# Optimization experiments

Hardware: AMD Instinct MI355X
Metric: run time of the kernel (lower is better)

## Reference

```python
import jax, jax.numpy as jnp
import numpy as np

B, T, N, F_IN, F_OUT = 8, 16, 512, 128, 64
NEG_INF = -9e15


def setup_inputs() -> dict:
    key = jax.random.key(0)
    k1, k2, k3, k4, k5 = jax.random.split(key, 5)
    x = jax.random.normal(k1, (B, T, N, F_IN), dtype=jnp.float32)
    # nn.Linear weights: FC_W [out, in], FC_a [1, 2*out], no bias
    W = jax.random.normal(k2, (F_OUT, F_IN), dtype=jnp.float32) * 0.05
    a = jax.random.normal(k3, (1, 2 * F_OUT), dtype=jnp.float32) * 0.05
    adj = jax.random.randint(k4, (N, N), 0, 2, dtype=jnp.int32)
    adj_we = jax.random.uniform(k5, (N, N), dtype=jnp.float32)
    return {"x": x, "W": W, "a": a, "adj": adj, "adj_we": adj_we}


def reference(x, W, a, adj, adj_we):
    fout = W.shape[0]
    # h = FC_W(input): [B,T,N,Fout]
    h = jnp.einsum("btnf,of->btno", x, W)
    # Additive GAT score decomposition: e[i,j] = LeakyReLU(a1.h_i + a2.h_j)
    # (equivalent to FC_a(cat([h_i, h_j])) without materializing [B,T,N,N,2F])
    a1 = a[0, :fout]
    a2 = a[0, fout:]
    src = jnp.einsum("btno,o->btn", h, a1)  # contribution of node i (repeated rows)
    dst = jnp.einsum("btno,o->btn", h, a2)  # contribution of node j (tiled rows)
    e = jax.nn.leaky_relu(src[..., :, None] + dst[..., None, :], negative_slope=0.01)
    # mask where adj <= 0, scale by edge weights, softmax over neighbors (dim=3)
    att = jnp.where(adj > 0, e, NEG_INF)
    att = att * adj_we
    att = jax.nn.softmax(att, axis=-1)
    # h_prime = attention @ h : [B,T,N,N] @ [B,T,N,Fout]
    return jnp.einsum("btij,btjo->btio", att, h)
```

## Files before the change

### kernel.cpp

```cpp
#include <hip/hip_runtime.h>
#include <hip/hip_bf16.h>

#define BTOT 128
#define NN   512
#define FIN  128
#define FOUT 64

typedef __attribute__((ext_vector_type(8))) short bf16x8;
typedef __attribute__((ext_vector_type(4))) float f32x4;

static __device__ inline ushort f2bf(float f) {
    __hip_bfloat16 h = __float2bfloat16(f);
    return *(ushort*)&h;
}
static __device__ inline float bf2f(ushort u) {
    uint v = (uint)u << 16;
    return __uint_as_float(v);
}

__global__ void k_prep(const float* __restrict__ W, const int* __restrict__ adj,
                       const float* __restrict__ we, ushort* __restrict__ Whi,
                       ushort* __restrict__ Wlo, ushort* __restrict__ cds) {
    int b = blockIdx.x;
    if (b >= 256) {
        int i = (b - 256) * 256 + threadIdx.x;
        float w = W[i];
        ushort hi = f2bf(w);
        Whi[i] = hi;
        Wlo[i] = f2bf(w - bf2f(hi));
        return;
    }
    int lin = (b * 256 + threadIdx.x) * 4;
    int i = lin >> 9, j0 = lin & 511;
    int4   a4 = *(const int4*)&adj[lin];
    float4 w4 = *(const float4*)&we[lin];
    ushort o[4];
#pragma unroll
    for (int e = 0; e < 4; ++e) {
        bool  cn = ((const int*)&a4)[e] > 0;
        float w  = ((const float*)&w4)[e];
        if (cn) {
            uint ub = __float_as_uint(w * 1.44269504f);
            uint tt = ub + 0xFFFFu + ((ub >> 17) & 1u);
            o[e] = (ushort)(((tt >> 17) << 1) | 1u);
        } else {
            o[e] = (w > 0.f) ? (ushort)0 : (ushort)1;
        }
    }
    int swz = ((((i >> 4) * 2 + (j0 >> 8)) * 8 + ((j0 >> 5) & 7)) << 9)
            + (((j0 >> 3) & 3) << 7) + ((i & 15) << 3) + (j0 & 7);
    *(uint2*)&cds[swz] = *(uint2*)&o[0];
}

__global__ void k_feat(const float* __restrict__ x, const ushort* __restrict__ Whi,
                       const ushort* __restrict__ Wlo, const float* __restrict__ a,
                       ushort* __restrict__ ht, float* __restrict__ srcv,
                       float* __restrict__ dstv) {
    const int t    = threadIdx.x;
    const int bid  = blockIdx.x;
    const int bt   = bid & 127;
    const int nt   = bid >> 7;
    const int wv   = t >> 6, lane = t & 63;
    const int r    = lane & 15;
    const int kc   = lane >> 4;
    const int n0   = nt * 64 + wv * 16;

    const float* xrow = x + ((long)bt * NN + n0 + r) * FIN;

    f32x4 acc[4] = {{0,0,0,0},{0,0,0,0},{0,0,0,0},{0,0,0,0}};

#pragma unroll
    for (int ks = 0; ks < 4; ++ks) {
        f32x4 xa = __builtin_nontemporal_load((const f32x4*)&xrow[ks * 32 + kc * 8]);
        f32x4 xb = __builtin_nontemporal_load((const f32x4*)&xrow[ks * 32 + kc * 8 + 4]);
        float xv[8] = {xa[0], xa[1], xa[2], xa[3], xb[0], xb[1], xb[2], xb[3]};
        bf16x8 Ahi, Alo;
#pragma unroll
        for (int e = 0; e < 8; ++e) {
            uint b = __float_as_uint(xv[e]);
            float hf = __uint_as_float(b & 0xFFFF0000u);
            Ahi[e] = (short)(b >> 16);
            float rr = xv[e] - hf;
            Alo[e] = (short)(__float_as_uint(rr) >> 16);
        }
#pragma unroll
        for (int g = 0; g < 4; ++g) {
            const int wo = (g * 16 + r) * FIN + ks * 32 + kc * 8;
            bf16x8 Bhi = *(const bf16x8*)&Whi[wo];
            bf16x8 Blo = *(const bf16x8*)&Wlo[wo];
            acc[g] = __builtin_amdgcn_mfma_f32_16x16x32_bf16(Ahi, Bhi, acc[g], 0, 0, 0);
            acc[g] = __builtin_amdgcn_mfma_f32_16x16x32_bf16(Alo, Bhi, acc[g], 0, 0, 0);
            acc[g] = __builtin_amdgcn_mfma_f32_16x16x32_bf16(Ahi, Blo, acc[g], 0, 0, 0);
        }
    }

    float a1g[4], a2g[4];
#pragma unroll
    for (int g = 0; g < 4; ++g) {
        a1g[g] = a[g * 16 + r];
        a2g[g] = a[FOUT + g * 16 + r];
    }
    f32x4 s1v = {0,0,0,0}, s2v = {0,0,0,0};
#pragma unroll
    for (int g = 0; g < 4; ++g)
#pragma unroll
        for (int reg = 0; reg < 4; ++reg) {
            s1v[reg] += acc[g][reg] * a1g[g];
            s2v[reg] += acc[g][reg] * a2g[g];
        }
#pragma unroll
    for (int off = 8; off; off >>= 1)
#pragma unroll
        for (int reg = 0; reg < 4; ++reg) {
            s1v[reg] += __shfl_down(s1v[reg], off, 16);
            s2v[reg] += __shfl_down(s2v[reg], off, 16);
        }
    if (r == 0) {
        float4 o1 = make_float4(s1v[0], s1v[1], s1v[2], s1v[3]);
        float4 o2 = make_float4(s2v[0], s2v[1], s2v[2], s2v[3]);
        *(float4*)&srcv[bt * NN + n0 + kc * 4] = o1;
        *(float4*)&dstv[bt * NN + n0 + kc * 4] = o2;
    }

#pragma unroll
    for (int g = 0; g < 4; ++g) {
        uint2 pk;
        pk.x = (uint)f2bf(acc[g][0]) | ((uint)f2bf(acc[g][1]) << 16);
        pk.y = (uint)f2bf(acc[g][2]) | ((uint)f2bf(acc[g][3]) << 16);
        *(uint2*)&ht[(long)bt * (FOUT * NN) + (g * 16 + r) * NN + n0 + kc * 4] = pk;
    }
}

static __device__ inline bf16x8 make_afrag(uint4 c, float4 d0, float4 d1, float si) {
    float dv[8] = {d0.x, d0.y, d0.z, d0.w, d1.x, d1.y, d1.z, d1.w};
    uint  cw[4] = {c.x, c.y, c.z, c.w};
    union { uint u[4]; bf16x8 v; } A;
#pragma unroll
    for (int q = 0; q < 4; ++q) {
        uint u = cw[q];
        float c0 = __uint_as_float((u << 16) & 0xFFFE0000u);
        float c1 = __uint_as_float(u & 0xFFFE0000u);
        float s0 = si + dv[2 * q],     lr0 = fmaxf(s0, 0.01f * s0);
        float s1 = si + dv[2 * q + 1], lr1 = fmaxf(s1, 0.01f * s1);
        float p0 = __builtin_amdgcn_exp2f(c0 * lr0);
        float p1 = __builtin_amdgcn_exp2f(c1 * lr1);
        p0 = (u & 1u)       ? p0 : 0.f;
        p1 = (u & 0x10000u) ? p1 : 0.f;
        A.u[q] = __builtin_amdgcn_perm(__float_as_uint(p1), __float_as_uint(p0),
                                       0x07060302u);
    }
    return A.v;
}

__global__ __launch_bounds__(256, 4)
void k_attn(const ushort* __restrict__ ht, const float* __restrict__ srcv,
            const float* __restrict__ dstv, const ushort* __restrict__ cds,
            float* __restrict__ out) {
    __shared__ ushort hs[64 * 256];
    __shared__ float dst_s[NN];

    const int t    = threadIdx.x;
    const int bid  = blockIdx.x;
    const int bt   = bid & 127;
    const int it   = bid >> 7;
    const int i0   = it << 6;
    const int lane = t & 63;
    const int wv   = t >> 6;
    const int r16  = lane & 15;
    const int kc   = lane >> 4;
    const int koff = kc * 8;
    const int xr   = r16 & 7;

    const int ri = i0 + wv * 16 + r16;
    const float si = srcv[bt * NN + ri];
    const ushort* cdb = cds + (((it * 4 + wv) * 2) << 12) + (lane << 3);
    const ushort* htb = ht + (long)bt * (FOUT * NN);

    for (int q = t; q < NN; q += 256) dst_s[q] = dstv[bt * NN + q];

    f32x4 ac0 = {0,0,0,0}, ac1 = {0,0,0,0}, ac2 = {0,0,0,0}, ac3 = {0,0,0,0},
          acd = {0,0,0,0};
    bf16x8 ones;
#pragma unroll
    for (int j = 0; j < 8; ++j) ones[j] = (short)0x3F80;

#pragma unroll
    for (int half = 0; half < 2; ++half) {
        uint4 cdv[8];
#pragma unroll
        for (int f = 0; f < 8; ++f)
            cdv[f] = *(const uint4*)&cdb[(half * 8 + f) << 9];

        __syncthreads();
#pragma unroll
        for (int q = 0; q < 8; ++q) {
            int idx = q * 256 + t;
            int o = idx >> 5, c8 = idx & 31;
            float4 v = *(const float4*)&htb[(o << 9) + (half << 8) + (c8 << 3)];
            *(float4*)&hs[(o << 8) + ((c8 ^ (o & 7)) << 3)] = v;
        }
        __syncthreads();

        const int jg = half * 256;
#pragma unroll
        for (int jtl = 0; jtl < 4; ++jtl) {
            const int jgc = jg + jtl * 64;
            float4 d00 = *(float4*)&dst_s[jgc + koff];
            float4 d01 = *(float4*)&dst_s[jgc + koff + 4];
            float4 d10 = *(float4*)&dst_s[jgc + 32 + koff];
            float4 d11 = *(float4*)&dst_s[jgc + 32 + koff + 4];

            bf16x8 A0 = make_afrag(cdv[2 * jtl],     d00, d01, si);
            bf16x8 A1 = make_afrag(cdv[2 * jtl + 1], d10, d11, si);

#pragma unroll
            for (int s2 = 0; s2 < 2; ++s2) {
                bf16x8 A = s2 ? A1 : A0;
                const int c8v = jtl * 8 + s2 * 4 + kc;
                const int cs  = (c8v ^ xr) << 3;
                bf16x8 b0 = *(bf16x8*)&hs[(( 0 + r16) << 8) + cs];
                bf16x8 b1 = *(bf16x8*)&hs[((16 + r16) << 8) + cs];
                bf16x8 b2 = *(bf16x8*)&hs[((32 + r16) << 8) + cs];
                bf16x8 b3 = *(bf16x8*)&hs[((48 + r16) << 8) + cs];
                __builtin_amdgcn_s_setprio(1);
                ac0 = __builtin_amdgcn_mfma_f32_16x16x32_bf16(A, b0, ac0, 0, 0, 0);
                ac1 = __builtin_amdgcn_mfma_f32_16x16x32_bf16(A, b1, ac1, 0, 0, 0);
                ac2 = __builtin_amdgcn_mfma_f32_16x16x32_bf16(A, b2, ac2, 0, 0, 0);
                ac3 = __builtin_amdgcn_mfma_f32_16x16x32_bf16(A, b3, ac3, 0, 0, 0);
                acd = __builtin_amdgcn_mfma_f32_16x16x32_bf16(A, ones, acd, 0, 0, 0);
                __builtin_amdgcn_s_setprio(0);
            }
        }
    }

    float* ob = out + ((long)bt * NN + i0 + wv * 16) * FOUT;
#pragma unroll
    for (int reg = 0; reg < 4; ++reg) {
        float inv = 1.0f / acd[reg];
        const int rw = (kc * 4 + reg) * FOUT + r16;
        __builtin_nontemporal_store(ac0[reg] * inv, &ob[rw +  0]);
        __builtin_nontemporal_store(ac1[reg] * inv, &ob[rw + 16]);
        __builtin_nontemporal_store(ac2[reg] * inv, &ob[rw + 32]);
        __builtin_nontemporal_store(ac3[reg] * inv, &ob[rw + 48]);
    }
}

extern "C" void kernel_launch(void* const* d_in, const int* in_sizes, int n_in,
                              void* d_out, int out_size, void* d_ws, size_t ws_size,
                              hipStream_t stream) {
    const float* x      = (const float*)d_in[0];
    const float* W      = (const float*)d_in[1];
    const float* a      = (const float*)d_in[2];
    const int*   adj    = (const int*)d_in[3];
    const float* adj_we = (const float*)d_in[4];
    float* out = (float*)d_out;

    ushort* Whi  = (ushort*)d_ws;
    ushort* Wlo  = Whi + FOUT * FIN;
    ushort* ht   = Wlo + FOUT * FIN;
    float*  srcv = (float*)(ht + BTOT * FOUT * NN);
    float*  dstv = srcv + BTOT * NN;
    ushort* cdsw = (ushort*)(dstv + BTOT * NN);

    hipLaunchKernelGGL(k_prep, dim3(288), dim3(256), 0, stream,
                       W, adj, adj_we, Whi, Wlo, cdsw);
    hipLaunchKernelGGL(k_feat, dim3(1024), dim3(256), 0, stream,
                       x, Whi, Wlo, a, ht, srcv, dstv);
    hipLaunchKernelGGL(k_attn, dim3(1024), dim3(256), 0, stream,
                       ht, srcv, dstv, cdsw, out);
}
```

Measured before the change: 46.57 us.

## Double-buffer h tiles in LDS via direct global-to-LDS loads across four stages

Splits the 512-column key loop into four 128-column stages with two LDS buffers. The next h tile is prefetched using global_load_lds (direct global-to-LDS, no register round trip) and the next adjacency/coefficient fragments are prefetched into registers while MFMAs run on the current buffer. The goal is to hide global load latency behind compute and shrink LDS use. It adds one barrier per stage and more live registers, and the XOR swizzle now happens on the global source addresses.

```diff
diff --git a/kernel.cpp b/kernel.cpp
--- a/kernel.cpp
+++ b/kernel.cpp
@@ -16,6 +16,12 @@
 static __device__ inline float bf2f(ushort u) {
     uint v = (uint)u << 16;
     return __uint_as_float(v);
+}
+
+static __device__ inline void gll16(const ushort* gsrc, ushort* ldst) {
+    __builtin_amdgcn_global_load_lds(
+        (const __attribute__((address_space(1))) uint*)gsrc,
+        (__attribute__((address_space(3))) uint*)ldst, 16, 0, 0);
 }
 
 __global__ void k_prep(const float* __restrict__ W, const int* __restrict__ adj,
@@ -156,7 +162,7 @@
 void k_attn(const ushort* __restrict__ ht, const float* __restrict__ srcv,
             const float* __restrict__ dstv, const ushort* __restrict__ cds,
             float* __restrict__ out) {
-    __shared__ ushort hs[64 * 256];
+    __shared__ ushort hs[2][64 * 128];
     __shared__ float dst_s[NN];
 
     const int t    = threadIdx.x;
@@ -176,6 +182,9 @@
     const ushort* cdb = cds + (((it * 4 + wv) * 2) << 12) + (lane << 3);
     const ushort* htb = ht + (long)bt * (FOUT * NN);
 
+    const int so  = t >> 4;
+    const int sgs = t & 15;
+
     for (int q = t; q < NN; q += 256) dst_s[q] = dstv[bt * NN + q];
 
     f32x4 ac0 = {0,0,0,0}, ac1 = {0,0,0,0}, ac2 = {0,0,0,0}, ac3 = {0,0,0,0},
@@ -184,44 +193,56 @@
 #pragma unroll
     for (int j = 0; j < 8; ++j) ones[j] = (short)0x3F80;
 
-#pragma unroll
-    for (int half = 0; half < 2; ++half) {
-        uint4 cdv[8];
-#pragma unroll
-        for (int f = 0; f < 8; ++f)
-            cdv[f] = *(const uint4*)&cdb[(half * 8 + f) << 9];
-
-        __syncthreads();
-#pragma unroll
-        for (int q = 0; q < 8; ++q) {
-            int idx = q * 256 + t;
-            int o = idx >> 5, c8 = idx & 31;
-            float4 v = *(const float4*)&htb[(o << 9) + (half << 8) + (c8 << 3)];
-            *(float4*)&hs[(o << 8) + ((c8 ^ (o & 7)) << 3)] = v;
-        }
-        __syncthreads();
-
-        const int jg = half * 256;
-#pragma unroll
-        for (int jtl = 0; jtl < 4; ++jtl) {
-            const int jgc = jg + jtl * 64;
-            float4 d00 = *(float4*)&dst_s[jgc + koff];
-            float4 d01 = *(float4*)&dst_s[jgc + koff + 4];
-            float4 d10 = *(float4*)&dst_s[jgc + 32 + koff];
-            float4 d11 = *(float4*)&dst_s[jgc + 32 + koff + 4];
-
-            bf16x8 A0 = make_afrag(cdv[2 * jtl],     d00, d01, si);
-            bf16x8 A1 = make_afrag(cdv[2 * jtl + 1], d10, d11, si);
+    uint4 cdc[4], cdn[4];
+#pragma unroll
+    for (int f = 0; f < 4; ++f) cdc[f] = *(const uint4*)&cdb[f << 9];
+
+#pragma unroll
+    for (int q = 0; q < 4; ++q) {
+        int idx = q * 256 + t;
+        int o = idx >> 4, gs = idx & 15;
+        gll16(htb + (o << 9) + ((gs ^ (o & 7)) << 3),
+              &hs[0][(q * 256 + (t & 0xC0)) * 8]);
+    }
+    __syncthreads();
+
+#pragma unroll
+    for (int qt = 0; qt < 4; ++qt) {
+        const int cur = qt & 1;
+
+        if (qt < 3) {
+#pragma unroll
+            for (int f = 0; f < 4; ++f)
+                cdn[f] = *(const uint4*)&cdb[(4 * (qt + 1) + f) << 9];
+#pragma unroll
+            for (int q = 0; q < 4; ++q) {
+                int idx = q * 256 + t;
+                int o = idx >> 4, gs = idx & 15;
+                gll16(htb + (o << 9) + ((qt + 1) << 7) + ((gs ^ (o & 7)) << 3),
+                      &hs[cur ^ 1][(q * 256 + (t & 0xC0)) * 8]);
+            }
+        }
+
+#pragma unroll
+        for (int j2 = 0; j2 < 2; ++j2) {
+            const int jb = qt * 128 + j2 * 64;
+            float4 d00 = *(float4*)&dst_s[jb + koff];
+            float4 d01 = *(float4*)&dst_s[jb + koff + 4];
+            float4 d10 = *(float4*)&dst_s[jb + 32 + koff];
+            float4 d11 = *(float4*)&dst_s[jb + 32 + koff + 4];
+
+            bf16x8 A0 = make_afrag(cdc[2 * j2],     d00, d01, si);
+            bf16x8 A1 = make_afrag(cdc[2 * j2 + 1], d10, d11, si);
 
 #pragma unroll
             for (int s2 = 0; s2 < 2; ++s2) {
                 bf16x8 A = s2 ? A1 : A0;
-                const int c8v = jtl * 8 + s2 * 4 + kc;
-                const int cs  = (c8v ^ xr) << 3;
-                bf16x8 b0 = *(bf16x8*)&hs[(( 0 + r16) << 8) + cs];
-                bf16x8 b1 = *(bf16x8*)&hs[((16 + r16) << 8) + cs];
-                bf16x8 b2 = *(bf16x8*)&hs[((32 + r16) << 8) + cs];
-                bf16x8 b3 = *(bf16x8*)&hs[((48 + r16) << 8) + cs];
+                const int g = j2 * 8 + s2 * 4 + kc;
+                const int cs = ((g ^ xr) << 3);
+                bf16x8 b0 = *(bf16x8*)&hs[cur][(( 0 + r16) << 7) + cs];
+                bf16x8 b1 = *(bf16x8*)&hs[cur][((16 + r16) << 7) + cs];
+                bf16x8 b2 = *(bf16x8*)&hs[cur][((32 + r16) << 7) + cs];
+                bf16x8 b3 = *(bf16x8*)&hs[cur][((48 + r16) << 7) + cs];
                 __builtin_amdgcn_s_setprio(1);
                 ac0 = __builtin_amdgcn_mfma_f32_16x16x32_bf16(A, b0, ac0, 0, 0, 0);
                 ac1 = __builtin_amdgcn_mfma_f32_16x16x32_bf16(A, b1, ac1, 0, 0, 0);
@@ -231,6 +252,10 @@
                 __builtin_amdgcn_s_setprio(0);
             }
         }
+
+        __syncthreads();
+#pragma unroll
+        for (int f = 0; f < 4; ++f) cdc[f] = cdn[f];
     }
 
     float* ob = out + ((long)bt * NN + i0 + wv * 16) * FOUT;
```

Measured after the change: 46.59 us. About the same (+0.0%).

## Fold adjacency preprocessing into feature kernel and hoist x loads ahead of MFMAs

Applied to the files above, without the earlier changes.

The adjacency/edge-weight encoding moves out of the prep kernel and into extra blocks of the feature kernel. That leaves only a tiny W split kernel on the critical path, and the adjacency work overlaps with the feature GEMM. The feature kernel now issues all x loads up front as ordinary cached loads instead of nontemporal ones, and converts them to bf16 hi/lo before the MFMA loop. It also gains launch bounds of 256 threads with 4 blocks. The cost is higher register pressure and a branch in k_feat that separates the two block roles.

```diff
diff --git a/kernel.cpp b/kernel.cpp
--- a/kernel.cpp
+++ b/kernel.cpp
@@ -18,46 +18,48 @@
     return __uint_as_float(v);
 }
 
-__global__ void k_prep(const float* __restrict__ W, const int* __restrict__ adj,
-                       const float* __restrict__ we, ushort* __restrict__ Whi,
-                       ushort* __restrict__ Wlo, ushort* __restrict__ cds) {
-    int b = blockIdx.x;
-    if (b >= 256) {
-        int i = (b - 256) * 256 + threadIdx.x;
-        float w = W[i];
-        ushort hi = f2bf(w);
-        Whi[i] = hi;
-        Wlo[i] = f2bf(w - bf2f(hi));
+__global__ void k_prep_w(const float* __restrict__ W, ushort* __restrict__ Whi,
+                         ushort* __restrict__ Wlo) {
+    int i = blockIdx.x * 256 + threadIdx.x;
+    float w = W[i];
+    ushort hi = f2bf(w);
+    Whi[i] = hi;
+    Wlo[i] = f2bf(w - bf2f(hi));
+}
+
+__global__ __launch_bounds__(256, 4)
+void k_feat(const float* __restrict__ x, const ushort* __restrict__ Whi,
+            const ushort* __restrict__ Wlo, const float* __restrict__ a,
+            ushort* __restrict__ ht, float* __restrict__ srcv,
+            float* __restrict__ dstv, const int* __restrict__ adj,
+            const float* __restrict__ we, ushort* __restrict__ cds) {
+    const int t   = threadIdx.x;
+    const int bid = blockIdx.x;
+
+    if (bid >= 1024) {
+        int lin = ((bid - 1024) * 256 + t) * 4;
+        int i = lin >> 9, j0 = lin & 511;
+        int4   a4 = *(const int4*)&adj[lin];
+        float4 w4 = *(const float4*)&we[lin];
+        ushort o[4];
+#pragma unroll
+        for (int e = 0; e < 4; ++e) {
+            bool  cn = ((const int*)&a4)[e] > 0;
+            float w  = ((const float*)&w4)[e];
+            if (cn) {
+                uint ub = __float_as_uint(w * 1.44269504f);
+                uint tt = ub + 0xFFFFu + ((ub >> 17) & 1u);
+                o[e] = (ushort)(((tt >> 17) << 1) | 1u);
+            } else {
+                o[e] = (w > 0.f) ? (ushort)0 : (ushort)1;
+            }
+        }
+        int swz = ((((i >> 4) * 2 + (j0 >> 8)) * 8 + ((j0 >> 5) & 7)) << 9)
+                + (((j0 >> 3) & 3) << 7) + ((i & 15) << 3) + (j0 & 7);
+        *(uint2*)&cds[swz] = *(uint2*)&o[0];
         return;
     }
-    int lin = (b * 256 + threadIdx.x) * 4;
-    int i = lin >> 9, j0 = lin & 511;
-    int4   a4 = *(const int4*)&adj[lin];
-    float4 w4 = *(const float4*)&we[lin];
-    ushort o[4];
-#pragma unroll
-    for (int e = 0; e < 4; ++e) {
-        bool  cn = ((const int*)&a4)[e] > 0;
-        float w  = ((const float*)&w4)[e];
-        if (cn) {
-            uint ub = __float_as_uint(w * 1.44269504f);
-            uint tt = ub + 0xFFFFu + ((ub >> 17) & 1u);
-            o[e] = (ushort)(((tt >> 17) << 1) | 1u);
-        } else {
-            o[e] = (w > 0.f) ? (ushort)0 : (ushort)1;
-        }
-    }
-    int swz = ((((i >> 4) * 2 + (j0 >> 8)) * 8 + ((j0 >> 5) & 7)) << 9)
-            + (((j0 >> 3) & 3) << 7) + ((i & 15) << 3) + (j0 & 7);
-    *(uint2*)&cds[swz] = *(uint2*)&o[0];
-}
-
-__global__ void k_feat(const float* __restrict__ x, const ushort* __restrict__ Whi,
-                       const ushort* __restrict__ Wlo, const float* __restrict__ a,
-                       ushort* __restrict__ ht, float* __restrict__ srcv,
-                       float* __restrict__ dstv) {
-    const int t    = threadIdx.x;
-    const int bid  = blockIdx.x;
+
     const int bt   = bid & 127;
     const int nt   = bid >> 7;
     const int wv   = t >> 6, lane = t & 63;
@@ -67,32 +69,37 @@
 
     const float* xrow = x + ((long)bt * NN + n0 + r) * FIN;
 
+    f32x4 xv8[8];
+#pragma unroll
+    for (int ks = 0; ks < 4; ++ks) {
+        xv8[2 * ks]     = *(const f32x4*)&xrow[ks * 32 + kc * 8];
+        xv8[2 * ks + 1] = *(const f32x4*)&xrow[ks * 32 + kc * 8 + 4];
+    }
+
+    bf16x8 Ahi[4], Alo[4];
+#pragma unroll
+    for (int ks = 0; ks < 4; ++ks)
+#pragma unroll
+        for (int e = 0; e < 8; ++e) {
+            float xe = (e < 4) ? xv8[2 * ks][e] : xv8[2 * ks + 1][e - 4];
+            uint b = __float_as_uint(xe);
+            Ahi[ks][e] = (short)(b >> 16);
+            float rr = xe - __uint_as_float(b & 0xFFFF0000u);
+            Alo[ks][e] = (short)(__float_as_uint(rr) >> 16);
+        }
+
     f32x4 acc[4] = {{0,0,0,0},{0,0,0,0},{0,0,0,0},{0,0,0,0}};
-
-#pragma unroll
-    for (int ks = 0; ks < 4; ++ks) {
-        f32x4 xa = __builtin_nontemporal_load((const f32x4*)&xrow[ks * 32 + kc * 8]);
-        f32x4 xb = __builtin_nontemporal_load((const f32x4*)&xrow[ks * 32 + kc * 8 + 4]);
-        float xv[8] = {xa[0], xa[1], xa[2], xa[3], xb[0], xb[1], xb[2], xb[3]};
-        bf16x8 Ahi, Alo;
-#pragma unroll
-        for (int e = 0; e < 8; ++e) {
-            uint b = __float_as_uint(xv[e]);
-            float hf = __uint_as_float(b & 0xFFFF0000u);
-            Ahi[e] = (short)(b >> 16);
-            float rr = xv[e] - hf;
-            Alo[e] = (short)(__float_as_uint(rr) >> 16);
-        }
+#pragma unroll
+    for (int ks = 0; ks < 4; ++ks)
 #pragma unroll
         for (int g = 0; g < 4; ++g) {
             const int wo = (g * 16 + r) * FIN + ks * 32 + kc * 8;
             bf16x8 Bhi = *(const bf16x8*)&Whi[wo];
             bf16x8 Blo = *(const bf16x8*)&Wlo[wo];
-            acc[g] = __builtin_amdgcn_mfma_f32_16x16x32_bf16(Ahi, Bhi, acc[g], 0, 0, 0);
-            acc[g] = __builtin_amdgcn_mfma_f32_16x16x32_bf16(Alo, Bhi, acc[g], 0, 0, 0);
-            acc[g] = __builtin_amdgcn_mfma_f32_16x16x32_bf16(Ahi, Blo, acc[g], 0, 0, 0);
-        }
-    }
+            acc[g] = __builtin_amdgcn_mfma_f32_16x16x32_bf16(Ahi[ks], Bhi, acc[g], 0, 0, 0);
+            acc[g] = __builtin_amdgcn_mfma_f32_16x16x32_bf16(Alo[ks], Bhi, acc[g], 0, 0, 0);
+            acc[g] = __builtin_amdgcn_mfma_f32_16x16x32_bf16(Ahi[ks], Blo, acc[g], 0, 0, 0);
+        }
 
     float a1g[4], a2g[4];
 #pragma unroll
@@ -262,10 +269,9 @@
     float*  dstv = srcv + BTOT * NN;
     ushort* cdsw = (ushort*)(dstv + BTOT * NN);
 
-    hipLaunchKernelGGL(k_prep, dim3(288), dim3(256), 0, stream,
-                       W, adj, adj_we, Whi, Wlo, cdsw);
-    hipLaunchKernelGGL(k_feat, dim3(1024), dim3(256), 0, stream,
-                       x, Whi, Wlo, a, ht, srcv, dstv);
+    hipLaunchKernelGGL(k_prep_w, dim3(32), dim3(256), 0, stream, W, Whi, Wlo);
+    hipLaunchKernelGGL(k_feat, dim3(1280), dim3(256), 0, stream,
+                       x, Whi, Wlo, a, ht, srcv, dstv, adj, adj_we, cdsw);
     hipLaunchKernelGGL(k_attn, dim3(1024), dim3(256), 0, stream,
                        ht, srcv, dstv, cdsw, out);
 }
```

Measured after the change: 46.82 us. No clear change (+0.5%).
